# Optimization experiments

Measured on AMD Instinct MI355X. Metric: run time of the kernel, lower is better.

Reference implementation:

```python
import jax, jax.numpy as jnp
import numpy as np

P = 16          # patch size
D = 256         # embed dim (complex channels)
L = 2           # depth (num blocks)
NE = 4          # num experts
FF = 1024       # ffn hidden = expand * D
B, T, C, IH, IW = 1, 8, 4, 256, 256
HP, WP = IH // P, IW // P


def setup_inputs():
    key = jax.random.key(0)
    ks = iter(jax.random.split(key, 40))
    r = lambda shape, s=0.02: jax.random.normal(next(ks), shape, jnp.float32) * s
    sD = 1.0 / np.sqrt(D)
    return {
        'x': jax.random.normal(next(ks), (B, T, C, IH, IW), jnp.float32),
        'dt': jax.random.uniform(next(ks), (B, T), jnp.float32, 0.1, 1.0),
        'Wenc': r((C * P * P, 2 * D)),
        'benc': jnp.zeros((2 * D,), jnp.float32),
        'Wdec': r((2 * D, C * P * P)),
        'bdec': jnp.zeros((C * P * P,), jnp.float32),
        'ln_sp_w': jnp.ones((L, 2 * D), jnp.float32),
        'ln_sp_b': jnp.zeros((L, 2 * D), jnp.float32),
        'conv_w': r((L, 2 * D, 2 * D, 3, 3)),
        'conv_b': jnp.zeros((L, 2 * D), jnp.float32),
        'E_re': r((L, D, D), sD), 'E_im': r((L, D, D), sD),
        'Ed_re': r((L, D, D), sD), 'Ed_im': r((L, D, D), sD),
        'Ws_re': r((L, D, D), sD), 'Ws_im': r((L, D, D), sD),
        'Wg': r((L, 2 * D, D)),
        'bg': jnp.zeros((L, D), jnp.float32),
        'lam_re': r((L, D), 1.0), 'lam_im': r((L, D), 1.0),
        'ln_t_w': jnp.ones((L, 2 * D), jnp.float32),
        'ln_t_b': jnp.zeros((L, 2 * D), jnp.float32),
        'Wr': r((L, 2 * D, NE)),
        'W1': r((L, NE, 2 * D, FF)),
        'W2': r((L, NE, FF, 2 * D)),
    }


def _ln(x, w, b):
    m = x.mean(-1, keepdims=True)
    v = ((x - m) ** 2).mean(-1, keepdims=True)
    return (x - m) * jax.lax.rsqrt(v + 1e-5) * w + b


def _block(z, h_prev, flux_prev, dt, bp):
    (ln_sp_w, ln_sp_b, conv_w, conv_b, E_re, E_im, Ed_re, Ed_im,
     Ws_re, Ws_im, Wg, bg, lam_re, lam_im, ln_t_w, ln_t_b, Wr, W1, W2) = bp
    Bq, Tq, Dq, H, W = z.shape
    # --- spatial process: LN + conv on concat(real, imag), complex residual ---
    zf = z.reshape(Bq * Tq, Dq, H, W)
    zr = jnp.concatenate([zf.real, zf.imag], axis=1)
    zn = _ln(zr.transpose(0, 2, 3, 1), ln_sp_w, ln_sp_b).transpose(0, 3, 1, 2)
    zs = jax.lax.conv_general_dilated(zn, conv_w, (1, 1), 'SAME',
                                      dimension_numbers=('NCHW', 'OIHW', 'NCHW'))
    zs = zs + conv_b[None, :, None, None]
    re, im = jnp.split(zs, 2, axis=1)
    x = (zf + (re + 1j * im)).reshape(Bq, Tq, Dq, H, W)
    # --- eigen-basis encode ---
    Eb = E_re + 1j * E_im
    x_eigen = jnp.einsum('btdhw,de->bthwe', x, Eb)   # [B,T,H,W,D] complex
    x_mean = x_eigen.mean(axis=(2, 3))               # [B,T,D] complex
    # --- sequential gated flux recurrence over T ---
    Ws = Ws_re + 1j * Ws_im
    def step(flux, xm):
        source = xm @ Ws
        feat = jnp.concatenate([xm.real, xm.imag], -1)
        gate = jax.nn.sigmoid(feat @ Wg + bg)        # real [B,D]
        new_flux = gate * flux + (1.0 - gate) * source
        return new_flux, (new_flux, source, gate)
    _, (flux_seq, source_seq, gate_seq) = jax.lax.scan(step, flux_prev, x_mean.transpose(1, 0, 2))
    flux_seq = flux_seq.transpose(1, 0, 2)
    source_seq = source_seq.transpose(1, 0, 2)
    gate_seq = gate_seq.transpose(1, 0, 2)
    g = gate_seq[:, :, None, None, :]
    forcing = x_eigen * g + source_seq[:, :, None, None, :] * (1.0 - g)
    # --- transition operators ---
    lam = -(jax.nn.softplus(lam_re) + 1e-2) + 1j * lam_im        # [D]
    op_decay = jnp.exp(lam[None, None, :] * dt[:, :, None])      # [B,T,D] complex
    op_forcing = (op_decay - 1.0) / lam
    a = jnp.broadcast_to(op_decay[:, :, None, None, :], forcing.shape)
    u = forcing * op_forcing[:, :, None, None, :]
    # --- parallel linear scan h_t = a_t * h_{t-1} + u_t along T ---
    def comb(c1, c2):
        a1, u1 = c1
        a2, u2 = c2
        return a1 * a2, u1 * a2 + u2
    _, h = jax.lax.associative_scan(comb, (a, u), axis=1)
    # as written in source: h_prev contribution is h_prev * op_decay at every t
    h = h + h_prev.reshape(Bq, 1, H, W, Dq) * a
    last_h = h[:, -1].reshape(Bq * H * W, 1, Dq)
    last_flux = flux_seq[:, -1]
    # --- eigen decode + temporal LN + MoE FFN ---
    Ed = Ed_re + 1j * Ed_im
    x_out = jnp.einsum('bthwe,ed->btdhw', h, Ed)
    xf = x_out.reshape(Bq * Tq, Dq, H, W)
    xr = jnp.concatenate([xf.real, xf.imag], axis=1)
    xn = _ln(xr.transpose(0, 2, 3, 1), ln_t_w, ln_t_b)           # [BT,H,W,2D]
    tok = xn.reshape(-1, 2 * Dq)
    probs = jax.nn.softmax(tok @ Wr, axis=-1)                    # [N,E]
    hid = jax.nn.gelu(jnp.einsum('nd,edf->nef', tok, W1))
    y = jnp.einsum('nef,efd,ne->nd', hid, W2, probs)             # [N,2D]
    xc = xn[..., :Dq] + 1j * xn[..., Dq:]
    delta = (y[..., :Dq] + 1j * y[..., Dq:]).reshape(Bq * Tq, H, W, Dq)
    x_cplx = (xc + delta).reshape(Bq, Tq, H, W, Dq).transpose(0, 1, 4, 2, 3)
    return x + x_cplx, last_h, last_flux


def _forward(x, dt, Wenc, benc, Wdec, bdec, ln_sp_w, ln_sp_b, conv_w, conv_b,
             E_re, E_im, Ed_re, Ed_im, Ws_re, Ws_im, Wg, bg, lam_re, lam_im,
             ln_t_w, ln_t_b, Wr, W1, W2):
    # encoder: patchify + linear -> complex latent [B,T,D,HP,WP]
    xp = x.reshape(B, T, C, HP, P, WP, P).transpose(0, 1, 3, 5, 2, 4, 6)
    xp = xp.reshape(B, T, HP, WP, C * P * P)
    ze = xp @ Wenc + benc                                        # [B,T,HP,WP,2D]
    z = (ze[..., :D] + 1j * ze[..., D:]).transpose(0, 1, 4, 2, 3)
    h_prev = jnp.zeros((B * HP * WP, 1, D), jnp.complex64)
    flux_prev = jnp.zeros((B, D), jnp.complex64)
    bparams = (ln_sp_w, ln_sp_b, conv_w, conv_b, E_re, E_im, Ed_re, Ed_im,
               Ws_re, Ws_im, Wg, bg, lam_re, lam_im, ln_t_w, ln_t_b, Wr, W1, W2)
    for i in range(L):
        bp = tuple(p[i] for p in bparams)
        z, h_prev, flux_prev = _block(z, h_prev, flux_prev, dt, bp)
    # decoder: linear + unpatchify (real output)
    zr = jnp.concatenate([z.real, z.imag], axis=2).transpose(0, 1, 3, 4, 2)
    yo = zr @ Wdec + bdec                                        # [B,T,HP,WP,C*P*P]
    out = yo.reshape(B, T, HP, WP, C, P, P).transpose(0, 1, 4, 2, 5, 3, 6)
    return out.reshape(B, T, C, IH, IW)


def reference(x, dt, Wenc, benc, Wdec, bdec, ln_sp_w, ln_sp_b, conv_w, conv_b,
              E_re, E_im, Ed_re, Ed_im, Ws_re, Ws_im, Wg, bg, lam_re, lam_im,
              ln_t_w, ln_t_b, Wr, W1, W2):
    return _forward(x, dt, Wenc, benc, Wdec, bdec, ln_sp_w, ln_sp_b, conv_w, conv_b,
                    E_re, E_im, Ed_re, Ed_im, Ws_re, Ws_im, Wg, bg, lam_re, lam_im,
                    ln_t_w, ln_t_b, Wr, W1, W2)
```

## Files before the change

kernel.cpp:

```cpp
#include <hip/hip_runtime.h>
#include <hip/hip_bf16.h>


#define TOKS 2048

typedef __bf16 bf16;
typedef __attribute__((ext_vector_type(8))) __bf16 bf16x8;
typedef __attribute__((ext_vector_type(4))) __bf16 bf16x4;
typedef __attribute__((ext_vector_type(4))) float f32x4;

enum GMode { EENC = 0, ECONV, ESQ, EMOE1, EMOE2, EDEC };

template <int MODE, int SPLIT>
__global__ __launch_bounds__(256) void mgemm_k(
    const bf16* __restrict__ A, const bf16* __restrict__ Bt,
    const float* __restrict__ bias, const float* __restrict__ addv,
    const float* __restrict__ scalev, float* __restrict__ C,
    bf16* __restrict__ C16, float* __restrict__ Cpart, int K, int N) {
  __shared__ __align__(16) bf16 As[64 * 40];
  __shared__ __align__(16) bf16 Bs[64 * 40];
  const int tid = threadIdx.x;
  const int bm = blockIdx.x * 64, bn = blockIdx.y * 64;
  const int lane = tid & 63, w = tid >> 6;
  const int wm = (w & 1) * 32, wn = (w >> 1) * 32;
  const int quad = lane >> 4, l16 = lane & 15;
  const int srow = tid >> 2, sko = (tid & 3) << 3;

  const int kbase = (SPLIT > 1) ? blockIdx.z * (K / SPLIT) : 0;
  const int kiter = K / (32 * SPLIT);
  if constexpr (MODE == EMOE1) Bt += (size_t)blockIdx.z * 524288;

  f32x4 acc[2][2] = {};

  int cv_t = 0, cv_h = 0, cv_w = 0;
  if constexpr (MODE == ECONV) {
    const int gm = bm + srow;
    cv_t = gm >> 8;
    cv_h = (gm >> 4) & 15;
    cv_w = gm & 15;
  }

  auto loadA = [&](int kt) -> bf16x8 {
    const int gk = kbase + kt * 32 + sko;
    if constexpr (MODE == ECONV) {
      const int s = gk >> 9, ci = gk & 511;
      const int kh = s / 3, kw = s - kh * 3;
      const int hh = cv_h + kh - 1, ww = cv_w + kw - 1;
      if (hh >= 0 && hh < 16 && ww >= 0 && ww < 16) {
        return *(const bf16x8*)&A[(size_t)(((cv_t << 8) + hh * 16 + ww) << 9) +
                                  ci];
      }
      bf16x8 zz;
#pragma unroll
      for (int q = 0; q < 8; q++) zz[q] = (bf16)0.0f;
      return zz;
    } else {
      return *(const bf16x8*)&A[(size_t)(bm + srow) * K + gk];
    }
  };
  auto loadB = [&](int kt) -> bf16x8 {
    return *(const bf16x8*)&Bt[(size_t)(bn + srow) * K + kbase + kt * 32 + sko];
  };

  bf16x8 pa = loadA(0), pb = loadB(0);
  for (int kt = 0; kt < kiter; kt++) {
    *(bf16x8*)&As[srow * 40 + sko] = pa;
    *(bf16x8*)&Bs[srow * 40 + sko] = pb;
    __syncthreads();
    if (kt + 1 < kiter) {
      pa = loadA(kt + 1);
      pb = loadB(kt + 1);
    }
    const bf16x8 a0 = *(const bf16x8*)&As[(wm + l16) * 40 + quad * 8];
    const bf16x8 a1 = *(const bf16x8*)&As[(wm + 16 + l16) * 40 + quad * 8];
    const bf16x8 b0 = *(const bf16x8*)&Bs[(wn + l16) * 40 + quad * 8];
    const bf16x8 b1 = *(const bf16x8*)&Bs[(wn + 16 + l16) * 40 + quad * 8];
    acc[0][0] = __builtin_amdgcn_mfma_f32_16x16x32_bf16(a0, b0, acc[0][0], 0, 0, 0);
    acc[0][1] = __builtin_amdgcn_mfma_f32_16x16x32_bf16(a0, b1, acc[0][1], 0, 0, 0);
    acc[1][0] = __builtin_amdgcn_mfma_f32_16x16x32_bf16(a1, b0, acc[1][0], 0, 0, 0);
    acc[1][1] = __builtin_amdgcn_mfma_f32_16x16x32_bf16(a1, b1, acc[1][1], 0, 0, 0);
    __syncthreads();
  }

#pragma unroll
  for (int i = 0; i < 2; i++) {
#pragma unroll
    for (int j = 0; j < 2; j++) {
#pragma unroll
      for (int r = 0; r < 4; r++) {
        const int gm = bm + wm + i * 16 + quad * 4 + r;
        const int gn = bn + wn + j * 16 + l16;
        const float v = acc[i][j][r];
        if constexpr (SPLIT > 1) {
          Cpart[(size_t)blockIdx.z * ((size_t)gridDim.x * 64 * N) +
                (size_t)gm * N + gn] = v;
        } else if constexpr (MODE == EENC) {
          C[(size_t)gm * 512 + gn] = v + bias[gn];
        } else if constexpr (MODE == ESQ) {
          C[(size_t)gm * 512 + gn] = v;
        } else if constexpr (MODE == EMOE1) {
          const float t = 0.7978845608028654f * (v + 0.044715f * v * v * v);
          const float g = 0.5f * v * (1.f + tanhf(t));
          const float p = scalev[gm * 4 + blockIdx.z];
          C16[(size_t)gm * 4096 + blockIdx.z * 1024 + gn] = (bf16)(p * g);
        } else {
          const int t = gm >> 8, hp = (gm >> 4) & 15, wp = gm & 15;
          const int c = gn >> 8, ph = (gn >> 4) & 15, pw = gn & 15;
          C[(size_t)(((t * 4 + c) * 256 + hp * 16 + ph) << 8) + wp * 16 + pw] =
              v + bias[gn];
        }
      }
    }
  }
}

__global__ __launch_bounds__(256) void conv_ep_k(
    const float* __restrict__ parts, const float* __restrict__ bias,
    const float* __restrict__ resid, float* __restrict__ xb,
    bf16* __restrict__ xb16) {
  const int i4 = (blockIdx.x * 256 + threadIdx.x) << 2;
  const int c = i4 & 511;
  const float4 p0 = *(const float4*)&parts[i4];
  const float4 p1 = *(const float4*)&parts[1048576 + i4];
  const float4 p2 = *(const float4*)&parts[2097152 + i4];
  const float4 p3 = *(const float4*)&parts[3145728 + i4];
  const float4 bi = *(const float4*)&bias[c];
  const float4 rz = *(const float4*)&resid[i4];
  float4 o;
  o.x = p0.x + p1.x + p2.x + p3.x + bi.x + rz.x;
  o.y = p0.y + p1.y + p2.y + p3.y + bi.y + rz.y;
  o.z = p0.z + p1.z + p2.z + p3.z + bi.z + rz.z;
  o.w = p0.w + p1.w + p2.w + p3.w + bi.w + rz.w;
  *(float4*)&xb[i4] = o;
  bf16x4 o16 = {(bf16)o.x, (bf16)o.y, (bf16)o.z, (bf16)o.w};
  *(bf16x4*)&xb16[i4] = o16;
}

__global__ __launch_bounds__(256) void addf_k(const float* __restrict__ xb,
                                              const float* __restrict__ zn,
                                              const float* __restrict__ parts,
                                              float* __restrict__ z,
                                              bf16* __restrict__ z16) {
  const int i4 = (blockIdx.x * 256 + threadIdx.x) << 2;
  const float4 a = *(const float4*)&xb[i4];
  const float4 b = *(const float4*)&zn[i4];
  const float4 p0 = *(const float4*)&parts[i4];
  const float4 p1 = *(const float4*)&parts[1048576 + i4];
  const float4 p2 = *(const float4*)&parts[2097152 + i4];
  const float4 p3 = *(const float4*)&parts[3145728 + i4];
  float4 o;
  o.x = a.x + b.x + p0.x + p1.x + p2.x + p3.x;
  o.y = a.y + b.y + p0.y + p1.y + p2.y + p3.y;
  o.z = a.z + b.z + p0.z + p1.z + p2.z + p3.z;
  o.w = a.w + b.w + p0.w + p1.w + p2.w + p3.w;
  *(float4*)&z[i4] = o;
  bf16x4 o16 = {(bf16)o.x, (bf16)o.y, (bf16)o.z, (bf16)o.w};
  *(bf16x4*)&z16[i4] = o16;
}

template <bool DO_PROBS>
__global__ __launch_bounds__(256) void ln_k(
    const float* __restrict__ in, const float* __restrict__ w,
    const float* __restrict__ b, const float* __restrict__ Wr,
    float* __restrict__ out, bf16* __restrict__ out16,
    float* __restrict__ probs) {
  const int wv = threadIdx.x >> 6, lane = threadIdx.x & 63;
  const int n = (blockIdx.x << 2) + wv;
  const float* row = in + (size_t)n * 512;
  float v[8];
  float s = 0.f, s2 = 0.f;
#pragma unroll
  for (int i = 0; i < 8; i++) {
    const float x = row[(i << 6) + lane];
    v[i] = x;
    s += x;
    s2 += x * x;
  }
#pragma unroll
  for (int off = 32; off > 0; off >>= 1) {
    s += __shfl_down(s, off);
    s2 += __shfl_down(s2, off);
  }
  s = __shfl(s, 0);
  s2 = __shfl(s2, 0);
  const float m = s * (1.f / 512.f);
  const float var = s2 * (1.f / 512.f) - m * m;
  const float r = rsqrtf(var + 1e-5f);
  float a0 = 0.f, a1 = 0.f, a2 = 0.f, a3 = 0.f;
#pragma unroll
  for (int i = 0; i < 8; i++) {
    const int c = (i << 6) + lane;
    const float o = (v[i] - m) * r * w[c] + b[c];
    out[(size_t)n * 512 + c] = o;
    out16[(size_t)n * 512 + c] = (bf16)o;
    if constexpr (DO_PROBS) {
      a0 += o * Wr[c * 4 + 0];
      a1 += o * Wr[c * 4 + 1];
      a2 += o * Wr[c * 4 + 2];
      a3 += o * Wr[c * 4 + 3];
    }
  }
  if constexpr (DO_PROBS) {
#pragma unroll
    for (int off = 32; off > 0; off >>= 1) {
      a0 += __shfl_down(a0, off);
      a1 += __shfl_down(a1, off);
      a2 += __shfl_down(a2, off);
      a3 += __shfl_down(a3, off);
    }
    if (lane == 0) {
      const float mx = fmaxf(fmaxf(a0, a1), fmaxf(a2, a3));
      const float e0 = expf(a0 - mx), e1 = expf(a1 - mx), e2 = expf(a2 - mx),
                  e3 = expf(a3 - mx);
      const float inv = 1.f / (e0 + e1 + e2 + e3);
      probs[n * 4 + 0] = e0 * inv;
      probs[n * 4 + 1] = e1 * inv;
      probs[n * 4 + 2] = e2 * inv;
      probs[n * 4 + 3] = e3 * inv;
    }
  }
}

__global__ __launch_bounds__(256) void cvt_enc_k(const float* __restrict__ x,
                                                 bf16* __restrict__ Ae) {
  const int id = blockIdx.x * 256 + threadIdx.x;
  const int n = id >> 7;
  const int kc = (id & 127) << 3;
  const int t = n >> 8, hp = (n >> 4) & 15, wp = n & 15;
  const int c = kc >> 8, ph = (kc >> 4) & 15, pw = kc & 15;
  const float* src =
      &x[(size_t)(((t * 4 + c) * 256 + hp * 16 + ph) << 8) + wp * 16 + pw];
  const float4 v0 = *(const float4*)src;
  const float4 v1 = *(const float4*)(src + 4);
  bf16* d = &Ae[(size_t)n * 1024 + kc];
  d[0] = (bf16)v0.x; d[1] = (bf16)v0.y; d[2] = (bf16)v0.z; d[3] = (bf16)v0.w;
  d[4] = (bf16)v1.x; d[5] = (bf16)v1.y; d[6] = (bf16)v1.z; d[7] = (bf16)v1.w;
}

__global__ __launch_bounds__(256) void cvtT_k(const float* __restrict__ src,
                                              bf16* __restrict__ dst, int K,
                                              int N) {
  __shared__ float tile[32][33];
  const size_t boff = (size_t)blockIdx.z * K * N;
  src += boff;
  dst += boff;
  const int k0 = blockIdx.x * 32, n0 = blockIdx.y * 32;
  const int tx = threadIdx.x & 31, ty = threadIdx.x >> 5;
#pragma unroll
  for (int r = 0; r < 4; r++)
    tile[ty + 8 * r][tx] = src[(size_t)(k0 + ty + 8 * r) * N + n0 + tx];
  __syncthreads();
#pragma unroll
  for (int r = 0; r < 4; r++)
    dst[(size_t)(n0 + ty + 8 * r) * K + k0 + tx] = (bf16)tile[tx][ty + 8 * r];
}

__global__ __launch_bounds__(256) void cvtW2_k(const float* __restrict__ W2,
                                               bf16* __restrict__ dst) {
  __shared__ float tile[32][33];
  const int z = blockIdx.z;
  const int l = z >> 2, e = z & 3;
  const float* src = W2 + (size_t)z * 524288;
  bf16* d = dst + (size_t)l * 512 * 4096 + e * 1024;
  const int k0 = blockIdx.x * 32, n0 = blockIdx.y * 32;
  const int tx = threadIdx.x & 31, ty = threadIdx.x >> 5;
#pragma unroll
  for (int r = 0; r < 4; r++)
    tile[ty + 8 * r][tx] = src[(size_t)(k0 + ty + 8 * r) * 512 + n0 + tx];
  __syncthreads();
#pragma unroll
  for (int r = 0; r < 4; r++)
    d[(size_t)(n0 + ty + 8 * r) * 4096 + k0 + tx] = (bf16)tile[tx][ty + 8 * r];
}

__global__ __launch_bounds__(256) void build_MEt_k(
    const float* __restrict__ E_re, const float* __restrict__ E_im,
    const float* __restrict__ Ed_re, const float* __restrict__ Ed_im,
    bf16* __restrict__ out) {
  const int z = blockIdx.z;
  const int l = z >> 1, which = z & 1;
  const float* Er = (which ? Ed_re : E_re) + l * 65536;
  const float* Ei = (which ? Ed_im : E_im) + l * 65536;
  bf16* dst = out + (size_t)z * 262144;
  const int idx = blockIdx.x * 256 + threadIdx.x;
  const int j = idx >> 9, k = idx & 511;
  const int kk = k & 255, jj = j & 255;
  const float er = Er[kk * 256 + jj], ei = Ei[kk * 256 + jj];
  const float v = (k < 256) ? ((j < 256) ? er : ei) : ((j < 256) ? -ei : er);
  dst[idx] = (bf16)v;
}

__global__ __launch_bounds__(256) void convBt16_k(const float* __restrict__ w,
                                                  bf16* __restrict__ dst) {
  const int l = blockIdx.z;
  const float* src = w + (size_t)l * 512 * 512 * 9;
  bf16* d = dst + (size_t)l * 512 * 4608;
  const int idx = blockIdx.x * 256 + threadIdx.x;
  const int co = idx / 4608;
  const int rem = idx - co * 4608;
  const int s = rem >> 9, ci = rem & 511;
  d[idx] = (bf16)src[(size_t)(co * 512 + ci) * 9 + s];
}

__global__ __launch_bounds__(256) void mean_k(const float* __restrict__ xe,
                                              float* __restrict__ xm) {
  const int t = blockIdx.x;
  const int c = blockIdx.y * 256 + threadIdx.x;
  float s = 0.f;
  for (int p = 0; p < 256; p++) s += xe[(size_t)((t << 8) + p) * 512 + c];
  xm[t * 512 + c] = s * (1.f / 256.f);
}

__global__ __launch_bounds__(256) void srcgate_k(
    const float* __restrict__ xm, const float* __restrict__ Wsr,
    const float* __restrict__ Wsi, const float* __restrict__ Wg,
    const float* __restrict__ bg, float* __restrict__ srcs,
    float* __restrict__ gts) {
  const int t = blockIdx.x, part = blockIdx.y, d = threadIdx.x;
  __shared__ float sxm[512];
  for (int c = d; c < 512; c += 256) sxm[c] = xm[t * 512 + c];
  __syncthreads();
  if (part == 0) {
    float s0 = 0.f, s1 = 0.f, s2 = 0.f, s3 = 0.f;
#pragma unroll 4
    for (int e = 0; e < 256; e += 4) {
      s0 += sxm[e + 0] * Wsr[(e + 0) * 256 + d] - sxm[256 + e + 0] * Wsi[(e + 0) * 256 + d];
      s1 += sxm[e + 1] * Wsr[(e + 1) * 256 + d] - sxm[256 + e + 1] * Wsi[(e + 1) * 256 + d];
      s2 += sxm[e + 2] * Wsr[(e + 2) * 256 + d] - sxm[256 + e + 2] * Wsi[(e + 2) * 256 + d];
      s3 += sxm[e + 3] * Wsr[(e + 3) * 256 + d] - sxm[256 + e + 3] * Wsi[(e + 3) * 256 + d];
    }
    srcs[t * 512 + d] = (s0 + s1) + (s2 + s3);
  } else if (part == 1) {
    float s0 = 0.f, s1 = 0.f, s2 = 0.f, s3 = 0.f;
#pragma unroll 4
    for (int e = 0; e < 256; e += 4) {
      s0 += sxm[e + 0] * Wsi[(e + 0) * 256 + d] + sxm[256 + e + 0] * Wsr[(e + 0) * 256 + d];
      s1 += sxm[e + 1] * Wsi[(e + 1) * 256 + d] + sxm[256 + e + 1] * Wsr[(e + 1) * 256 + d];
      s2 += sxm[e + 2] * Wsi[(e + 2) * 256 + d] + sxm[256 + e + 2] * Wsr[(e + 2) * 256 + d];
      s3 += sxm[e + 3] * Wsi[(e + 3) * 256 + d] + sxm[256 + e + 3] * Wsr[(e + 3) * 256 + d];
    }
    srcs[t * 512 + 256 + d] = (s0 + s1) + (s2 + s3);
  } else {
    float s0 = 0.f, s1 = 0.f, s2 = 0.f, s3 = 0.f;
#pragma unroll 4
    for (int c = 0; c < 512; c += 4) {
      s0 += sxm[c + 0] * Wg[(c + 0) * 256 + d];
      s1 += sxm[c + 1] * Wg[(c + 1) * 256 + d];
      s2 += sxm[c + 2] * Wg[(c + 2) * 256 + d];
      s3 += sxm[c + 3] * Wg[(c + 3) * 256 + d];
    }
    const float ga = (s0 + s1) + (s2 + s3) + bg[d];
    gts[t * 256 + d] = 1.f / (1.f + expf(-ga));
  }
}

__global__ __launch_bounds__(256) void fluxrec_k(
    const float* __restrict__ srcs, const float* __restrict__ gts,
    const float* __restrict__ lamre, const float* __restrict__ lamim,
    const float* __restrict__ dt, float* __restrict__ flux,
    float* __restrict__ opd, float* __restrict__ opf) {
  const int d = threadIdx.x;
  float fr = flux[d], fi = flux[256 + d];
  const float lr0 = lamre[d];
  const float sp = (lr0 > 20.f) ? lr0 : log1pf(expf(lr0));
  const float lre = -(sp + 0.01f);
  const float lim = lamim[d];
  const float den = lre * lre + lim * lim;
#pragma unroll
  for (int t = 0; t < 8; t++) {
    const float g = gts[t * 256 + d];
    const float sr = srcs[t * 512 + d], si = srcs[t * 512 + 256 + d];
    fr = g * fr + (1.f - g) * sr;
    fi = g * fi + (1.f - g) * si;
    const float dtv = dt[t];
    const float er = expf(lre * dtv);
    const float odr = er * cosf(lim * dtv);
    const float odi = er * sinf(lim * dtv);
    opd[t * 512 + d] = odr;
    opd[t * 512 + 256 + d] = odi;
    const float nr = odr - 1.f, ni = odi;
    opf[t * 512 + d] = (nr * lre + ni * lim) / den;
    opf[t * 512 + 256 + d] = (ni * lre - nr * lim) / den;
  }
  flux[d] = fr;
  flux[256 + d] = fi;
}

__global__ __launch_bounds__(256) void time_scan_k(
    const float* __restrict__ xe, const float* __restrict__ gts,
    const float* __restrict__ srcs, const float* __restrict__ opd,
    const float* __restrict__ opf, bf16* __restrict__ hout16,
    float* __restrict__ hprev) {
  const int d = threadIdx.x;
  const int p = blockIdx.x;
  float hr = 0.f, hi = 0.f;
  const float hpr = hprev[p * 512 + d], hpi = hprev[p * 512 + 256 + d];
  float o7r = 0.f, o7i = 0.f;
  for (int t = 0; t < 8; t++) {
    const size_t base = (size_t)((t << 8) + p) * 512;
    const float xr = xe[base + d], xi = xe[base + 256 + d];
    const float g = gts[t * 256 + d];
    const float sr = srcs[t * 512 + d], si = srcs[t * 512 + 256 + d];
    const float fr = xr * g + sr * (1.f - g);
    const float fi = xi * g + si * (1.f - g);
    const float ofr = opf[t * 512 + d], ofi = opf[t * 512 + 256 + d];
    const float ur = fr * ofr - fi * ofi;
    const float ui = fr * ofi + fi * ofr;
    const float ar = opd[t * 512 + d], ai = opd[t * 512 + 256 + d];
    const float nhr = ur + ar * hr - ai * hi;
    const float nhi = ui + ar * hi + ai * hr;
    hr = nhr;
    hi = nhi;
    const float outr = hr + ar * hpr - ai * hpi;
    const float outi = hi + ar * hpi + ai * hpr;
    hout16[base + d] = (bf16)outr;
    hout16[base + 256 + d] = (bf16)outi;
    if (t == 7) {
      o7r = outr;
      o7i = outi;
    }
  }
  hprev[p * 512 + d] = o7r;
  hprev[p * 512 + 256 + d] = o7i;
}

extern "C" void kernel_launch(void* const* d_in, const int* in_sizes, int n_in,
                              void* d_out, int out_size, void* d_ws,
                              size_t ws_size, hipStream_t stream) {
  const float* x_in = (const float*)d_in[0];
  const float* dt = (const float*)d_in[1];
  const float* Wenc = (const float*)d_in[2];
  const float* benc = (const float*)d_in[3];
  const float* Wdec = (const float*)d_in[4];
  const float* bdec = (const float*)d_in[5];
  const float* ln_sp_w = (const float*)d_in[6];
  const float* ln_sp_b = (const float*)d_in[7];
  const float* conv_w = (const float*)d_in[8];
  const float* conv_b = (const float*)d_in[9];
  const float* E_re = (const float*)d_in[10];
  const float* E_im = (const float*)d_in[11];
  const float* Ed_re = (const float*)d_in[12];
  const float* Ed_im = (const float*)d_in[13];
  const float* Ws_re = (const float*)d_in[14];
  const float* Ws_im = (const float*)d_in[15];
  const float* Wg = (const float*)d_in[16];
  const float* bg = (const float*)d_in[17];
  const float* lam_re = (const float*)d_in[18];
  const float* lam_im = (const float*)d_in[19];
  const float* ln_t_w = (const float*)d_in[20];
  const float* ln_t_b = (const float*)d_in[21];
  const float* Wr = (const float*)d_in[22];
  const float* W1 = (const float*)d_in[23];
  const float* W2 = (const float*)d_in[24];
  float* out = (float*)d_out;

  float* ws = (float*)d_ws;
  size_t off = 0;
  auto allocf = [&](size_t n) {
    float* p = ws + off;
    off += n;
    return p;
  };
  auto allocb = [&](size_t n) {
    bf16* p = (bf16*)(ws + off);
    off += n / 2;
    return p;
  };
  float* z = allocf((size_t)TOKS * 512);
  float* zn = allocf((size_t)TOKS * 512);
  float* xb = allocf((size_t)TOKS * 512);
  float* xe = allocf((size_t)TOKS * 512);
  float* parts = allocf((size_t)4 * TOKS * 512);
  float* hprev = allocf(256 * 512);
  float* flux = allocf(512);
  float* xm = allocf(8 * 512);
  float* srcs = allocf(8 * 512);
  float* gts = allocf(8 * 256);
  float* opd = allocf(8 * 512);
  float* opf = allocf(8 * 512);
  float* probs = allocf((size_t)TOKS * 4);
  bf16* zn16 = allocb((size_t)TOKS * 512);
  bf16* xb16 = allocb((size_t)TOKS * 512);
  bf16* z16 = allocb((size_t)TOKS * 512);
  bf16* hb16 = allocb((size_t)TOKS * 512);
  bf16* hid16 = allocb((size_t)TOKS * 4096);
  bf16* Aenc16 = allocb((size_t)TOKS * 1024);
  bf16* WencT = allocb((size_t)512 * 1024);
  bf16* WdecT = allocb((size_t)1024 * 512);
  bf16* MEt = allocb((size_t)4 * 512 * 512);
  bf16* convBt = allocb((size_t)2 * 512 * 4608);
  bf16* W1T = allocb((size_t)8 * 1024 * 512);
  bf16* W2Tc = allocb((size_t)2 * 512 * 4096);

  hipMemsetAsync(hprev, 0, 256 * 512 * sizeof(float), stream);
  hipMemsetAsync(flux, 0, 512 * sizeof(float), stream);

  cvt_enc_k<<<1024, 256, 0, stream>>>(x_in, Aenc16);
  cvtT_k<<<dim3(32, 16, 1), 256, 0, stream>>>(Wenc, WencT, 1024, 512);
  cvtT_k<<<dim3(16, 32, 1), 256, 0, stream>>>(Wdec, WdecT, 512, 1024);
  cvtT_k<<<dim3(16, 32, 8), 256, 0, stream>>>(W1, W1T, 512, 1024);
  cvtW2_k<<<dim3(32, 16, 8), 256, 0, stream>>>(W2, W2Tc);
  build_MEt_k<<<dim3(1024, 1, 4), 256, 0, stream>>>(E_re, E_im, Ed_re, Ed_im,
                                                    MEt);
  convBt16_k<<<dim3(9216, 1, 2), 256, 0, stream>>>(conv_w, convBt);

  mgemm_k<EENC, 1><<<dim3(32, 8), 256, 0, stream>>>(
      Aenc16, WencT, benc, nullptr, nullptr, z, nullptr, nullptr, 1024, 512);

  for (int l = 0; l < 2; l++) {
    ln_k<false><<<512, 256, 0, stream>>>(z, ln_sp_w + l * 512,
                                         ln_sp_b + l * 512, nullptr, zn, zn16,
                                         nullptr);
    mgemm_k<ECONV, 4><<<dim3(32, 8, 4), 256, 0, stream>>>(
        zn16, convBt + (size_t)l * 512 * 4608, nullptr, nullptr, nullptr,
        nullptr, nullptr, parts, 4608, 512);
    conv_ep_k<<<1024, 256, 0, stream>>>(parts, conv_b + l * 512, z, xb, xb16);
    mgemm_k<ESQ, 1><<<dim3(32, 8), 256, 0, stream>>>(
        xb16, MEt + (size_t)(l * 2) * 262144, nullptr, nullptr, nullptr, xe,
        nullptr, nullptr, 512, 512);
    mean_k<<<dim3(8, 2), 256, 0, stream>>>(xe, xm);
    srcgate_k<<<dim3(8, 3), 256, 0, stream>>>(
        xm, Ws_re + l * 65536, Ws_im + l * 65536, Wg + l * 131072, bg + l * 256,
        srcs, gts);
    fluxrec_k<<<1, 256, 0, stream>>>(srcs, gts, lam_re + l * 256,
                                     lam_im + l * 256, dt, flux, opd, opf);
    time_scan_k<<<256, 256, 0, stream>>>(xe, gts, srcs, opd, opf, hb16, hprev);
    mgemm_k<ESQ, 1><<<dim3(32, 8), 256, 0, stream>>>(
        hb16, MEt + (size_t)(l * 2 + 1) * 262144, nullptr, nullptr, nullptr, xe,
        nullptr, nullptr, 512, 512);
    ln_k<true><<<512, 256, 0, stream>>>(xe, ln_t_w + l * 512, ln_t_b + l * 512,
                                        Wr + l * 2048, zn, zn16, probs);
    mgemm_k<EMOE1, 1><<<dim3(32, 16, 4), 256, 0, stream>>>(
        zn16, W1T + (size_t)l * 4 * 524288, nullptr, nullptr, probs, nullptr,
        hid16, nullptr, 512, 1024);
    mgemm_k<EMOE2, 4><<<dim3(32, 8, 4), 256, 0, stream>>>(
        hid16, W2Tc + (size_t)l * 512 * 4096, nullptr, nullptr, nullptr,
        nullptr, nullptr, parts, 4096, 512);
    addf_k<<<1024, 256, 0, stream>>>(xb, zn, parts, z, z16);
  }

  mgemm_k<EDEC, 1><<<dim3(32, 16), 256, 0, stream>>>(
      z16, WdecT, bdec, nullptr, nullptr, out, nullptr, nullptr, 512, 1024);
}
```

Baseline: 498.4 us.

## Use 128x128 GEMM tiles for big matmuls and fuse small setup kernels

Adds a 128x128-tile MFMA GEMM variant with 4x4 accumulators per wave for the conv, MoE up and MoE down projections, raising data reuse per LDS load. Merges all weight/input conversion kernels into a single launch, folds the token mean into the source-gate kernel, and computes the decay operators inside the time scan, dropping the flux recurrence, hprev memset and several launches. The larger tiles reduce block count and raise register use, which may lower occupancy.

```diff
diff --git a/kernel.cpp b/kernel.cpp
--- a/kernel.cpp
+++ b/kernel.cpp
@@ -11,12 +11,10 @@
 
 enum GMode { EENC = 0, ECONV, ESQ, EMOE1, EMOE2, EDEC };
 
-template <int MODE, int SPLIT>
+template <int MODE>
 __global__ __launch_bounds__(256) void mgemm_k(
     const bf16* __restrict__ A, const bf16* __restrict__ Bt,
-    const float* __restrict__ bias, const float* __restrict__ addv,
-    const float* __restrict__ scalev, float* __restrict__ C,
-    bf16* __restrict__ C16, float* __restrict__ Cpart, int K, int N) {
+    const float* __restrict__ bias, float* __restrict__ C, int K, int N) {
   __shared__ __align__(16) bf16 As[64 * 40];
   __shared__ __align__(16) bf16 Bs[64 * 40];
   const int tid = threadIdx.x;
@@ -26,40 +24,14 @@
   const int quad = lane >> 4, l16 = lane & 15;
   const int srow = tid >> 2, sko = (tid & 3) << 3;
 
-  const int kbase = (SPLIT > 1) ? blockIdx.z * (K / SPLIT) : 0;
-  const int kiter = K / (32 * SPLIT);
-  if constexpr (MODE == EMOE1) Bt += (size_t)blockIdx.z * 524288;
-
   f32x4 acc[2][2] = {};
-
-  int cv_t = 0, cv_h = 0, cv_w = 0;
-  if constexpr (MODE == ECONV) {
-    const int gm = bm + srow;
-    cv_t = gm >> 8;
-    cv_h = (gm >> 4) & 15;
-    cv_w = gm & 15;
-  }
+  const int kiter = K / 32;
 
   auto loadA = [&](int kt) -> bf16x8 {
-    const int gk = kbase + kt * 32 + sko;
-    if constexpr (MODE == ECONV) {
-      const int s = gk >> 9, ci = gk & 511;
-      const int kh = s / 3, kw = s - kh * 3;
-      const int hh = cv_h + kh - 1, ww = cv_w + kw - 1;
-      if (hh >= 0 && hh < 16 && ww >= 0 && ww < 16) {
-        return *(const bf16x8*)&A[(size_t)(((cv_t << 8) + hh * 16 + ww) << 9) +
-                                  ci];
-      }
-      bf16x8 zz;
-#pragma unroll
-      for (int q = 0; q < 8; q++) zz[q] = (bf16)0.0f;
-      return zz;
-    } else {
-      return *(const bf16x8*)&A[(size_t)(bm + srow) * K + gk];
-    }
+    return *(const bf16x8*)&A[(size_t)(bm + srow) * K + kt * 32 + sko];
   };
   auto loadB = [&](int kt) -> bf16x8 {
-    return *(const bf16x8*)&Bt[(size_t)(bn + srow) * K + kbase + kt * 32 + sko];
+    return *(const bf16x8*)&Bt[(size_t)(bn + srow) * K + kt * 32 + sko];
   };
 
   bf16x8 pa = loadA(0), pb = loadB(0);
@@ -91,23 +63,117 @@
         const int gm = bm + wm + i * 16 + quad * 4 + r;
         const int gn = bn + wn + j * 16 + l16;
         const float v = acc[i][j][r];
-        if constexpr (SPLIT > 1) {
-          Cpart[(size_t)blockIdx.z * ((size_t)gridDim.x * 64 * N) +
-                (size_t)gm * N + gn] = v;
-        } else if constexpr (MODE == EENC) {
+        if constexpr (MODE == EENC) {
           C[(size_t)gm * 512 + gn] = v + bias[gn];
         } else if constexpr (MODE == ESQ) {
           C[(size_t)gm * 512 + gn] = v;
-        } else if constexpr (MODE == EMOE1) {
-          const float t = 0.7978845608028654f * (v + 0.044715f * v * v * v);
-          const float g = 0.5f * v * (1.f + tanhf(t));
-          const float p = scalev[gm * 4 + blockIdx.z];
-          C16[(size_t)gm * 4096 + blockIdx.z * 1024 + gn] = (bf16)(p * g);
         } else {
           const int t = gm >> 8, hp = (gm >> 4) & 15, wp = gm & 15;
           const int c = gn >> 8, ph = (gn >> 4) & 15, pw = gn & 15;
           C[(size_t)(((t * 4 + c) * 256 + hp * 16 + ph) << 8) + wp * 16 + pw] =
               v + bias[gn];
+        }
+      }
+    }
+  }
+}
+
+template <int MODE, int SPLIT>
+__global__ __launch_bounds__(256) void mgemm2_k(
+    const bf16* __restrict__ A, const bf16* __restrict__ Bt,
+    const float* __restrict__ scalev, bf16* __restrict__ C16,
+    float* __restrict__ Cpart, int K, int N) {
+  __shared__ __align__(16) bf16 As[128 * 40];
+  __shared__ __align__(16) bf16 Bs[128 * 40];
+  const int tid = threadIdx.x;
+  const int bm = blockIdx.x * 128, bn = blockIdx.y * 128;
+  const int lane = tid & 63, w = tid >> 6;
+  const int wm = (w & 1) * 64, wn = (w >> 1) * 64;
+  const int quad = lane >> 4, l16 = lane & 15;
+  const int srow = tid >> 1, sko = (tid & 1) << 4;
+
+  const int kbase = (SPLIT > 1) ? blockIdx.z * (K / SPLIT) : 0;
+  const int kiter = K / (32 * SPLIT);
+  if constexpr (MODE == EMOE1) Bt += (size_t)blockIdx.z * 524288;
+
+  f32x4 acc[4][4] = {};
+
+  int cv_t = 0, cv_h = 0, cv_w = 0;
+  if constexpr (MODE == ECONV) {
+    const int gm = bm + srow;
+    cv_t = gm >> 8;
+    cv_h = (gm >> 4) & 15;
+    cv_w = gm & 15;
+  }
+
+  auto loadA = [&](int kt, int half) -> bf16x8 {
+    const int gk = kbase + kt * 32 + sko + half * 8;
+    if constexpr (MODE == ECONV) {
+      const int s = gk >> 9, ci = gk & 511;
+      const int kh = s / 3, kw = s - kh * 3;
+      const int hh = cv_h + kh - 1, ww = cv_w + kw - 1;
+      if (hh >= 0 && hh < 16 && ww >= 0 && ww < 16)
+        return *(const bf16x8*)&A[(size_t)(((cv_t << 8) + hh * 16 + ww) << 9) +
+                                  ci];
+      bf16x8 zz;
+#pragma unroll
+      for (int q = 0; q < 8; q++) zz[q] = (bf16)0.0f;
+      return zz;
+    } else {
+      return *(const bf16x8*)&A[(size_t)(bm + srow) * K + gk];
+    }
+  };
+  auto loadB = [&](int kt, int half) -> bf16x8 {
+    return *(const bf16x8*)&Bt[(size_t)(bn + srow) * K + kbase + kt * 32 + sko +
+                               half * 8];
+  };
+
+  bf16x8 pa0 = loadA(0, 0), pa1 = loadA(0, 1);
+  bf16x8 pb0 = loadB(0, 0), pb1 = loadB(0, 1);
+  for (int kt = 0; kt < kiter; kt++) {
+    *(bf16x8*)&As[srow * 40 + sko] = pa0;
+    *(bf16x8*)&As[srow * 40 + sko + 8] = pa1;
+    *(bf16x8*)&Bs[srow * 40 + sko] = pb0;
+    *(bf16x8*)&Bs[srow * 40 + sko + 8] = pb1;
+    __syncthreads();
+    if (kt + 1 < kiter) {
+      pa0 = loadA(kt + 1, 0);
+      pa1 = loadA(kt + 1, 1);
+      pb0 = loadB(kt + 1, 0);
+      pb1 = loadB(kt + 1, 1);
+    }
+    bf16x8 af[4], bfr[4];
+#pragma unroll
+    for (int i = 0; i < 4; i++)
+      af[i] = *(const bf16x8*)&As[(wm + i * 16 + l16) * 40 + quad * 8];
+#pragma unroll
+    for (int j = 0; j < 4; j++)
+      bfr[j] = *(const bf16x8*)&Bs[(wn + j * 16 + l16) * 40 + quad * 8];
+#pragma unroll
+    for (int i = 0; i < 4; i++)
+#pragma unroll
+      for (int j = 0; j < 4; j++)
+        acc[i][j] =
+            __builtin_amdgcn_mfma_f32_16x16x32_bf16(af[i], bfr[j], acc[i][j], 0, 0, 0);
+    __syncthreads();
+  }
+
+#pragma unroll
+  for (int i = 0; i < 4; i++) {
+#pragma unroll
+    for (int j = 0; j < 4; j++) {
+#pragma unroll
+      for (int r = 0; r < 4; r++) {
+        const int gm = bm + wm + i * 16 + quad * 4 + r;
+        const int gn = bn + wn + j * 16 + l16;
+        const float v = acc[i][j][r];
+        if constexpr (SPLIT > 1) {
+          Cpart[(size_t)blockIdx.z * 1048576 + (size_t)gm * 512 + gn] = v;
+        } else {
+          const float t = 0.7978845608028654f * (v + 0.044715f * v * v * v);
+          const float g = 0.5f * v * (1.f + tanhf(t));
+          const float p = scalev[gm * 4 + blockIdx.z];
+          C16[(size_t)gm * 4096 + blockIdx.z * 1024 + gn] = (bf16)(p * g);
         }
       }
     }
@@ -221,104 +287,121 @@
   }
 }
 
-__global__ __launch_bounds__(256) void cvt_enc_k(const float* __restrict__ x,
-                                                 bf16* __restrict__ Ae) {
-  const int id = blockIdx.x * 256 + threadIdx.x;
-  const int n = id >> 7;
-  const int kc = (id & 127) << 3;
-  const int t = n >> 8, hp = (n >> 4) & 15, wp = n & 15;
-  const int c = kc >> 8, ph = (kc >> 4) & 15, pw = kc & 15;
-  const float* src =
-      &x[(size_t)(((t * 4 + c) * 256 + hp * 16 + ph) << 8) + wp * 16 + pw];
-  const float4 v0 = *(const float4*)src;
-  const float4 v1 = *(const float4*)(src + 4);
-  bf16* d = &Ae[(size_t)n * 1024 + kc];
-  d[0] = (bf16)v0.x; d[1] = (bf16)v0.y; d[2] = (bf16)v0.z; d[3] = (bf16)v0.w;
-  d[4] = (bf16)v1.x; d[5] = (bf16)v1.y; d[6] = (bf16)v1.z; d[7] = (bf16)v1.w;
-}
-
-__global__ __launch_bounds__(256) void cvtT_k(const float* __restrict__ src,
-                                              bf16* __restrict__ dst, int K,
-                                              int N) {
+__global__ __launch_bounds__(256) void cvt_all_k(
+    const float* __restrict__ x, const float* __restrict__ Wenc,
+    const float* __restrict__ Wdec, const float* __restrict__ W1,
+    const float* __restrict__ W2, const float* __restrict__ E_re,
+    const float* __restrict__ E_im, const float* __restrict__ Ed_re,
+    const float* __restrict__ Ed_im, const float* __restrict__ conv_w,
+    bf16* __restrict__ Ae, bf16* __restrict__ WencT, bf16* __restrict__ WdecT,
+    bf16* __restrict__ W1T, bf16* __restrict__ W2Tc, bf16* __restrict__ MEt,
+    bf16* __restrict__ convBt) {
   __shared__ float tile[32][33];
-  const size_t boff = (size_t)blockIdx.z * K * N;
-  src += boff;
-  dst += boff;
-  const int k0 = blockIdx.x * 32, n0 = blockIdx.y * 32;
-  const int tx = threadIdx.x & 31, ty = threadIdx.x >> 5;
-#pragma unroll
-  for (int r = 0; r < 4; r++)
-    tile[ty + 8 * r][tx] = src[(size_t)(k0 + ty + 8 * r) * N + n0 + tx];
-  __syncthreads();
-#pragma unroll
-  for (int r = 0; r < 4; r++)
-    dst[(size_t)(n0 + ty + 8 * r) * K + k0 + tx] = (bf16)tile[tx][ty + 8 * r];
-}
-
-__global__ __launch_bounds__(256) void cvtW2_k(const float* __restrict__ W2,
-                                               bf16* __restrict__ dst) {
-  __shared__ float tile[32][33];
-  const int z = blockIdx.z;
-  const int l = z >> 2, e = z & 3;
-  const float* src = W2 + (size_t)z * 524288;
-  bf16* d = dst + (size_t)l * 512 * 4096 + e * 1024;
-  const int k0 = blockIdx.x * 32, n0 = blockIdx.y * 32;
-  const int tx = threadIdx.x & 31, ty = threadIdx.x >> 5;
-#pragma unroll
-  for (int r = 0; r < 4; r++)
-    tile[ty + 8 * r][tx] = src[(size_t)(k0 + ty + 8 * r) * 512 + n0 + tx];
-  __syncthreads();
-#pragma unroll
-  for (int r = 0; r < 4; r++)
-    d[(size_t)(n0 + ty + 8 * r) * 4096 + k0 + tx] = (bf16)tile[tx][ty + 8 * r];
-}
-
-__global__ __launch_bounds__(256) void build_MEt_k(
-    const float* __restrict__ E_re, const float* __restrict__ E_im,
-    const float* __restrict__ Ed_re, const float* __restrict__ Ed_im,
-    bf16* __restrict__ out) {
-  const int z = blockIdx.z;
-  const int l = z >> 1, which = z & 1;
-  const float* Er = (which ? Ed_re : E_re) + l * 65536;
-  const float* Ei = (which ? Ed_im : E_im) + l * 65536;
-  bf16* dst = out + (size_t)z * 262144;
-  const int idx = blockIdx.x * 256 + threadIdx.x;
-  const int j = idx >> 9, k = idx & 511;
-  const int kk = k & 255, jj = j & 255;
-  const float er = Er[kk * 256 + jj], ei = Ei[kk * 256 + jj];
-  const float v = (k < 256) ? ((j < 256) ? er : ei) : ((j < 256) ? -ei : er);
-  dst[idx] = (bf16)v;
-}
-
-__global__ __launch_bounds__(256) void convBt16_k(const float* __restrict__ w,
-                                                  bf16* __restrict__ dst) {
-  const int l = blockIdx.z;
-  const float* src = w + (size_t)l * 512 * 512 * 9;
-  bf16* d = dst + (size_t)l * 512 * 4608;
-  const int idx = blockIdx.x * 256 + threadIdx.x;
-  const int co = idx / 4608;
-  const int rem = idx - co * 4608;
-  const int s = rem >> 9, ci = rem & 511;
-  d[idx] = (bf16)src[(size_t)(co * 512 + ci) * 9 + s];
-}
-
-__global__ __launch_bounds__(256) void mean_k(const float* __restrict__ xe,
-                                              float* __restrict__ xm) {
-  const int t = blockIdx.x;
-  const int c = blockIdx.y * 256 + threadIdx.x;
-  float s = 0.f;
-  for (int p = 0; p < 256; p++) s += xe[(size_t)((t << 8) + p) * 512 + c];
-  xm[t * 512 + c] = s * (1.f / 256.f);
+  const int tid = threadIdx.x;
+  int b = blockIdx.x;
+  const int tx = tid & 31, ty = tid >> 5;
+  auto tpose = [&](const float* src, bf16* dst, int K, int N, int dstride,
+                   int k0, int n0) {
+#pragma unroll
+    for (int r = 0; r < 4; r++)
+      tile[ty + 8 * r][tx] = src[(size_t)(k0 + ty + 8 * r) * N + n0 + tx];
+    __syncthreads();
+#pragma unroll
+    for (int r = 0; r < 4; r++)
+      dst[(size_t)(n0 + ty + 8 * r) * dstride + k0 + tx] =
+          (bf16)tile[tx][ty + 8 * r];
+  };
+  if (b < 1024) {
+    const int id = b * 256 + tid;
+    const int n = id >> 7;
+    const int kc = (id & 127) << 3;
+    const int t = n >> 8, hp = (n >> 4) & 15, wp = n & 15;
+    const int c = kc >> 8, ph = (kc >> 4) & 15, pw = kc & 15;
+    const float* src =
+        &x[(size_t)(((t * 4 + c) * 256 + hp * 16 + ph) << 8) + wp * 16 + pw];
+    const float4 v0 = *(const float4*)src;
+    const float4 v1 = *(const float4*)(src + 4);
+    bf16* d = &Ae[(size_t)n * 1024 + kc];
+    d[0] = (bf16)v0.x; d[1] = (bf16)v0.y; d[2] = (bf16)v0.z; d[3] = (bf16)v0.w;
+    d[4] = (bf16)v1.x; d[5] = (bf16)v1.y; d[6] = (bf16)v1.z; d[7] = (bf16)v1.w;
+    return;
+  }
+  b -= 1024;
+  if (b < 512) {
+    tpose(Wenc, WencT, 1024, 512, 1024, (b & 31) * 32, (b >> 5) * 32);
+    return;
+  }
+  b -= 512;
+  if (b < 512) {
+    tpose(Wdec, WdecT, 512, 1024, 512, (b & 15) * 32, (b >> 4) * 32);
+    return;
+  }
+  b -= 512;
+  if (b < 4096) {
+    const int z = b >> 9, rem = b & 511;
+    tpose(W1 + (size_t)z * 524288, W1T + (size_t)z * 524288, 512, 1024, 512,
+          (rem & 15) * 32, (rem >> 4) * 32);
+    return;
+  }
+  b -= 4096;
+  if (b < 4096) {
+    const int z = b >> 9, rem = b & 511;
+    const int l = z >> 2, e = z & 3;
+    tpose(W2 + (size_t)z * 524288, W2Tc + (size_t)l * 2097152 + e * 1024, 1024,
+          512, 4096, (rem & 31) * 32, (rem >> 5) * 32);
+    return;
+  }
+  b -= 4096;
+  if (b < 4096) {
+    const int z = b >> 10;
+    const int l = z >> 1, which = z & 1;
+    const float* Er = (which ? Ed_re : E_re) + l * 65536;
+    const float* Ei = (which ? Ed_im : E_im) + l * 65536;
+    bf16* dst = MEt + (size_t)z * 262144;
+    const int idx = (b & 1023) * 256 + tid;
+    const int j = idx >> 9, k = idx & 511;
+    const int kk = k & 255, jj = j & 255;
+    const float er = Er[kk * 256 + jj], ei = Ei[kk * 256 + jj];
+    const float v = (k < 256) ? ((j < 256) ? er : ei) : ((j < 256) ? -ei : er);
+    dst[idx] = (bf16)v;
+    return;
+  }
+  b -= 4096;
+  {
+    const int z = b / 2304;
+    const int rem = b - z * 2304;
+    const float* src = conv_w + (size_t)z * 2359296;
+    bf16* d = convBt + (size_t)z * 2359296;
+    const int idx = (rem * 256 + tid) << 2;
+    const int co = idx / 4608;
+    const int r2 = idx - co * 4608;
+    const int s = r2 >> 9, ci = r2 & 511;
+    bf16x4 o;
+#pragma unroll
+    for (int q = 0; q < 4; q++)
+      o[q] = (bf16)src[(size_t)(co * 512 + ci + q) * 9 + s];
+    *(bf16x4*)&d[idx] = o;
+  }
 }
 
 __global__ __launch_bounds__(256) void srcgate_k(
-    const float* __restrict__ xm, const float* __restrict__ Wsr,
+    const float* __restrict__ xe, const float* __restrict__ Wsr,
     const float* __restrict__ Wsi, const float* __restrict__ Wg,
     const float* __restrict__ bg, float* __restrict__ srcs,
     float* __restrict__ gts) {
   const int t = blockIdx.x, part = blockIdx.y, d = threadIdx.x;
   __shared__ float sxm[512];
-  for (int c = d; c < 512; c += 256) sxm[c] = xm[t * 512 + c];
+  for (int c = d; c < 512; c += 256) {
+    const float* col = xe + (size_t)(t << 8) * 512 + c;
+    float s0 = 0.f, s1 = 0.f, s2 = 0.f, s3 = 0.f;
+    for (int p = 0; p < 256; p += 4) {
+      s0 += col[(size_t)(p + 0) * 512];
+      s1 += col[(size_t)(p + 1) * 512];
+      s2 += col[(size_t)(p + 2) * 512];
+      s3 += col[(size_t)(p + 3) * 512];
+    }
+    sxm[c] = ((s0 + s1) + (s2 + s3)) * (1.f / 256.f);
+  }
   __syncthreads();
   if (part == 0) {
     float s0 = 0.f, s1 = 0.f, s2 = 0.f, s3 = 0.f;
@@ -354,48 +437,40 @@
   }
 }
 
-__global__ __launch_bounds__(256) void fluxrec_k(
-    const float* __restrict__ srcs, const float* __restrict__ gts,
-    const float* __restrict__ lamre, const float* __restrict__ lamim,
-    const float* __restrict__ dt, float* __restrict__ flux,
-    float* __restrict__ opd, float* __restrict__ opf) {
+template <bool FIRST>
+__global__ __launch_bounds__(256) void time_scan_k(
+    const float* __restrict__ xe, const float* __restrict__ gts,
+    const float* __restrict__ srcs, const float* __restrict__ lamre,
+    const float* __restrict__ lamim, const float* __restrict__ dt,
+    bf16* __restrict__ hout16, float* __restrict__ hprev) {
   const int d = threadIdx.x;
-  float fr = flux[d], fi = flux[256 + d];
+  const int p = blockIdx.x;
   const float lr0 = lamre[d];
   const float sp = (lr0 > 20.f) ? lr0 : log1pf(expf(lr0));
   const float lre = -(sp + 0.01f);
   const float lim = lamim[d];
   const float den = lre * lre + lim * lim;
+  float ar[8], ai[8], ofr[8], ofi[8];
 #pragma unroll
   for (int t = 0; t < 8; t++) {
-    const float g = gts[t * 256 + d];
-    const float sr = srcs[t * 512 + d], si = srcs[t * 512 + 256 + d];
-    fr = g * fr + (1.f - g) * sr;
-    fi = g * fi + (1.f - g) * si;
     const float dtv = dt[t];
     const float er = expf(lre * dtv);
     const float odr = er * cosf(lim * dtv);
     const float odi = er * sinf(lim * dtv);
-    opd[t * 512 + d] = odr;
-    opd[t * 512 + 256 + d] = odi;
+    ar[t] = odr;
+    ai[t] = odi;
     const float nr = odr - 1.f, ni = odi;
-    opf[t * 512 + d] = (nr * lre + ni * lim) / den;
-    opf[t * 512 + 256 + d] = (ni * lre - nr * lim) / den;
-  }
-  flux[d] = fr;
-  flux[256 + d] = fi;
-}
-
-__global__ __launch_bounds__(256) void time_scan_k(
-    const float* __restrict__ xe, const float* __restrict__ gts,
-    const float* __restrict__ srcs, const float* __restrict__ opd,
-    const float* __restrict__ opf, bf16* __restrict__ hout16,
-    float* __restrict__ hprev) {
-  const int d = threadIdx.x;
-  const int p = blockIdx.x;
+    ofr[t] = (nr * lre + ni * lim) / den;
+    ofi[t] = (ni * lre - nr * lim) / den;
+  }
   float hr = 0.f, hi = 0.f;
-  const float hpr = hprev[p * 512 + d], hpi = hprev[p * 512 + 256 + d];
+  float hpr = 0.f, hpi = 0.f;
+  if constexpr (!FIRST) {
+    hpr = hprev[p * 512 + d];
+    hpi = hprev[p * 512 + 256 + d];
+  }
   float o7r = 0.f, o7i = 0.f;
+#pragma unroll
   for (int t = 0; t < 8; t++) {
     const size_t base = (size_t)((t << 8) + p) * 512;
     const float xr = xe[base + d], xi = xe[base + 256 + d];
@@ -403,16 +478,14 @@
     const float sr = srcs[t * 512 + d], si = srcs[t * 512 + 256 + d];
     const float fr = xr * g + sr * (1.f - g);
     const float fi = xi * g + si * (1.f - g);
-    const float ofr = opf[t * 512 + d], ofi = opf[t * 512 + 256 + d];
-    const float ur = fr * ofr - fi * ofi;
-    const float ui = fr * ofi + fi * ofr;
-    const float ar = opd[t * 512 + d], ai = opd[t * 512 + 256 + d];
-    const float nhr = ur + ar * hr - ai * hi;
-    const float nhi = ui + ar * hi + ai * hr;
+    const float ur = fr * ofr[t] - fi * ofi[t];
+    const float ui = fr * ofi[t] + fi * ofr[t];
+    const float nhr = ur + ar[t] * hr - ai[t] * hi;
+    const float nhi = ui + ar[t] * hi + ai[t] * hr;
     hr = nhr;
     hi = nhi;
-    const float outr = hr + ar * hpr - ai * hpi;
-    const float outi = hi + ar * hpi + ai * hpr;
+    const float outr = hr + ar[t] * hpr - ai[t] * hpi;
+    const float outi = hi + ar[t] * hpi + ai[t] * hpr;
     hout16[base + d] = (bf16)outr;
     hout16[base + 256 + d] = (bf16)outi;
     if (t == 7) {
@@ -472,12 +545,8 @@
   float* xe = allocf((size_t)TOKS * 512);
   float* parts = allocf((size_t)4 * TOKS * 512);
   float* hprev = allocf(256 * 512);
-  float* flux = allocf(512);
-  float* xm = allocf(8 * 512);
   float* srcs = allocf(8 * 512);
   float* gts = allocf(8 * 256);
-  float* opd = allocf(8 * 512);
-  float* opf = allocf(8 * 512);
   float* probs = allocf((size_t)TOKS * 4);
   bf16* zn16 = allocb((size_t)TOKS * 512);
   bf16* xb16 = allocb((size_t)TOKS * 512);
@@ -492,53 +561,44 @@
   bf16* W1T = allocb((size_t)8 * 1024 * 512);
   bf16* W2Tc = allocb((size_t)2 * 512 * 4096);
 
-  hipMemsetAsync(hprev, 0, 256 * 512 * sizeof(float), stream);
-  hipMemsetAsync(flux, 0, 512 * sizeof(float), stream);
-
-  cvt_enc_k<<<1024, 256, 0, stream>>>(x_in, Aenc16);
-  cvtT_k<<<dim3(32, 16, 1), 256, 0, stream>>>(Wenc, WencT, 1024, 512);
-  cvtT_k<<<dim3(16, 32, 1), 256, 0, stream>>>(Wdec, WdecT, 512, 1024);
-  cvtT_k<<<dim3(16, 32, 8), 256, 0, stream>>>(W1, W1T, 512, 1024);
-  cvtW2_k<<<dim3(32, 16, 8), 256, 0, stream>>>(W2, W2Tc);
-  build_MEt_k<<<dim3(1024, 1, 4), 256, 0, stream>>>(E_re, E_im, Ed_re, Ed_im,
-                                                    MEt);
-  convBt16_k<<<dim3(9216, 1, 2), 256, 0, stream>>>(conv_w, convBt);
-
-  mgemm_k<EENC, 1><<<dim3(32, 8), 256, 0, stream>>>(
-      Aenc16, WencT, benc, nullptr, nullptr, z, nullptr, nullptr, 1024, 512);
+  cvt_all_k<<<18944, 256, 0, stream>>>(x_in, Wenc, Wdec, W1, W2, E_re, E_im,
+                                       Ed_re, Ed_im, conv_w, Aenc16, WencT,
+                                       WdecT, W1T, W2Tc, MEt, convBt);
+
+  mgemm_k<EENC><<<dim3(32, 8), 256, 0, stream>>>(Aenc16, WencT, benc, z, 1024,
+                                                 512);
 
   for (int l = 0; l < 2; l++) {
     ln_k<false><<<512, 256, 0, stream>>>(z, ln_sp_w + l * 512,
                                          ln_sp_b + l * 512, nullptr, zn, zn16,
                                          nullptr);
-    mgemm_k<ECONV, 4><<<dim3(32, 8, 4), 256, 0, stream>>>(
-        zn16, convBt + (size_t)l * 512 * 4608, nullptr, nullptr, nullptr,
-        nullptr, nullptr, parts, 4608, 512);
+    mgemm2_k<ECONV, 4><<<dim3(16, 4, 4), 256, 0, stream>>>(
+        zn16, convBt + (size_t)l * 512 * 4608, nullptr, nullptr, parts, 4608,
+        512);
     conv_ep_k<<<1024, 256, 0, stream>>>(parts, conv_b + l * 512, z, xb, xb16);
-    mgemm_k<ESQ, 1><<<dim3(32, 8), 256, 0, stream>>>(
-        xb16, MEt + (size_t)(l * 2) * 262144, nullptr, nullptr, nullptr, xe,
-        nullptr, nullptr, 512, 512);
-    mean_k<<<dim3(8, 2), 256, 0, stream>>>(xe, xm);
-    srcgate_k<<<dim3(8, 3), 256, 0, stream>>>(
-        xm, Ws_re + l * 65536, Ws_im + l * 65536, Wg + l * 131072, bg + l * 256,
-        srcs, gts);
-    fluxrec_k<<<1, 256, 0, stream>>>(srcs, gts, lam_re + l * 256,
-                                     lam_im + l * 256, dt, flux, opd, opf);
-    time_scan_k<<<256, 256, 0, stream>>>(xe, gts, srcs, opd, opf, hb16, hprev);
-    mgemm_k<ESQ, 1><<<dim3(32, 8), 256, 0, stream>>>(
-        hb16, MEt + (size_t)(l * 2 + 1) * 262144, nullptr, nullptr, nullptr, xe,
-        nullptr, nullptr, 512, 512);
+    mgemm_k<ESQ><<<dim3(32, 8), 256, 0, stream>>>(
+        xb16, MEt + (size_t)(l * 2) * 262144, nullptr, xe, 512, 512);
+    srcgate_k<<<dim3(8, 3), 256, 0, stream>>>(xe, Ws_re + l * 65536,
+                                              Ws_im + l * 65536,
+                                              Wg + l * 131072, bg + l * 256,
+                                              srcs, gts);
+    if (l == 0)
+      time_scan_k<true><<<256, 256, 0, stream>>>(
+          xe, gts, srcs, lam_re, lam_im, dt, hb16, hprev);
+    else
+      time_scan_k<false><<<256, 256, 0, stream>>>(
+          xe, gts, srcs, lam_re + 256, lam_im + 256, dt, hb16, hprev);
+    mgemm_k<ESQ><<<dim3(32, 8), 256, 0, stream>>>(
+        hb16, MEt + (size_t)(l * 2 + 1) * 262144, nullptr, xe, 512, 512);
     ln_k<true><<<512, 256, 0, stream>>>(xe, ln_t_w + l * 512, ln_t_b + l * 512,
                                         Wr + l * 2048, zn, zn16, probs);
-    mgemm_k<EMOE1, 1><<<dim3(32, 16, 4), 256, 0, stream>>>(
-        zn16, W1T + (size_t)l * 4 * 524288, nullptr, nullptr, probs, nullptr,
-        hid16, nullptr, 512, 1024);
-    mgemm_k<EMOE2, 4><<<dim3(32, 8, 4), 256, 0, stream>>>(
-        hid16, W2Tc + (size_t)l * 512 * 4096, nullptr, nullptr, nullptr,
-        nullptr, nullptr, parts, 4096, 512);
+    mgemm2_k<EMOE1, 1><<<dim3(16, 8, 4), 256, 0, stream>>>(
+        zn16, W1T + (size_t)l * 2097152, probs, hid16, nullptr, 512, 1024);
+    mgemm2_k<EMOE2, 4><<<dim3(16, 4, 4), 256, 0, stream>>>(
+        hid16, W2Tc + (size_t)l * 2097152, nullptr, nullptr, parts, 4096, 512);
     addf_k<<<1024, 256, 0, stream>>>(xb, zn, parts, z, z16);
   }
 
-  mgemm_k<EDEC, 1><<<dim3(32, 16), 256, 0, stream>>>(
-      z16, WdecT, bdec, nullptr, nullptr, out, nullptr, nullptr, 512, 1024);
-}
+  mgemm_k<EDEC><<<dim3(32, 16), 256, 0, stream>>>(z16, WdecT, bdec, out, 512,
+                                                  1024);
+}
```

New measurement: 495.1 us. Within noise of the previous version (-0.7%).
